# Optimization experiments

Measured on AMD Instinct MI355X. Metric: run time of the kernel, lower is better.

The kernel has to match this reference:

```python
import jax, jax.numpy as jnp
import numpy as np

# Intersection(mode='product'):
#   a_fk = a @ feats.T            # [Na, K]
#   b_fk = b @ feats.T            # [Nb, K]
#   mask = (a_fk[:,None,:] > 0) & (b_fk[None,:,:] > 0)
#   result = sum_k (a_fk[:,None,:] * b_fk[None,:,:]) * mask   # [Na, Nb]
# For the product op, (x*y)*[x>0 & y>0] == relu(x)*relu(y) elementwise
# (any term with a non-positive factor is zeroed either way), so the
# broadcast+mask+reduce collapses exactly into a GEMM over relu'd scores.

def setup_inputs() -> dict:
    key = jax.random.key(0)
    k1, k2, k3 = jax.random.split(key, 3)
    a = jax.random.normal(k1, (1024, 2048), dtype=jnp.float32)
    b = jax.random.normal(k2, (1024, 2048), dtype=jnp.float32)
    feats = jax.random.normal(k3, (128, 2048), dtype=jnp.float32)
    return {"a": a, "b": b, "feats": feats}

def reference(a, b, feats):
    a_fk = a @ feats.T            # [Na, K]
    b_fk = b @ feats.T            # [Nb, K]
    # masked product-intersection reduced over K; identical math to the
    # broadcast (Na, Nb, K) -> sum formulation of the torch module.
    return jnp.einsum('ak,bk->ab', jax.nn.relu(a_fk), jax.nn.relu(b_fk))
```

## Files before the change

### kernel.cpp

```cpp
#include <hip/hip_runtime.h>


typedef __attribute__((ext_vector_type(8))) __bf16 bf16x8;
typedef __attribute__((ext_vector_type(4))) __bf16 bf16x4;
typedef __attribute__((ext_vector_type(4))) float floatx4;

#define KD     2048
#define NF     128
#define NA     1024
#define NPART  8
#define KSL    256
#define FKN    (2048 * 128)

static __device__ inline bf16x4 cvt4(float4 u) {
    bf16x4 s;
    s[0] = (__bf16)u.x; s[1] = (__bf16)u.y; s[2] = (__bf16)u.z; s[3] = (__bf16)u.w;
    return s;
}

__global__ __launch_bounds__(256) void gemm1_part8(const float* __restrict__ A,
                                                   const float* __restrict__ B,
                                                   const float* __restrict__ F,
                                                   float* __restrict__ part) {
    __shared__ __bf16 Xs[32 * 72];
    __shared__ __bf16 Fs[128 * 72];

    const int t    = threadIdx.x;
    const int m0   = blockIdx.x * 32;
    const int s    = blockIdx.y;
    const int k0   = s * KSL;
    const float* src = (m0 < NA) ? (A + (size_t)m0 * KD)
                                 : (B + (size_t)(m0 - NA) * KD);

    const int lane = t & 63;
    const int w    = t >> 6;
    const int ln   = lane & 15;
    const int quad = lane >> 4;
    const int q8   = quad * 8;

    floatx4 acc[2][2];
#pragma unroll
    for (int mt = 0; mt < 2; mt++)
#pragma unroll
        for (int nt = 0; nt < 2; nt++)
            acc[mt][nt] = (floatx4){0.f, 0.f, 0.f, 0.f};

    const int srow = t >> 4;
    const int scol = (t & 15) * 4;
    const float* xp0 = src + (size_t)srow * KD        + (k0 + scol);
    const float* xp1 = src + (size_t)(srow + 16) * KD + (k0 + scol);
    const float* fp  = F   + (size_t)srow * KD        + (k0 + scol);

    float4 x0 = *(const float4*)(xp0);
    float4 x1 = *(const float4*)(xp1);
    float4 fa[8];
#pragma unroll
    for (int i = 0; i < 8; i++)
        fa[i] = *(const float4*)(fp + (size_t)i * 16 * KD);

#pragma unroll
    for (int kk = 0; kk < KSL; kk += 64) {
        *(bf16x4*)&Xs[srow * 72 + scol]        = cvt4(x0);
        *(bf16x4*)&Xs[(srow + 16) * 72 + scol] = cvt4(x1);
#pragma unroll
        for (int i = 0; i < 8; i++)
            *(bf16x4*)&Fs[(i * 16 + srow) * 72 + scol] = cvt4(fa[i]);
        __syncthreads();

        if (kk + 64 < KSL) {
            x0 = *(const float4*)(xp0 + kk + 64);
            x1 = *(const float4*)(xp1 + kk + 64);
#pragma unroll
            for (int i = 0; i < 8; i++)
                fa[i] = *(const float4*)(fp + (size_t)i * 16 * KD + kk + 64);
        }

#pragma unroll
        for (int sub = 0; sub < 64; sub += 32) {
            bf16x8 bfrag[2];
#pragma unroll
            for (int nt = 0; nt < 2; nt++)
                bfrag[nt] = *(const bf16x8*)&Fs[(w * 32 + nt * 16 + ln) * 72 + sub + q8];
#pragma unroll
            for (int mt = 0; mt < 2; mt++) {
                bf16x8 af = *(const bf16x8*)&Xs[(mt * 16 + ln) * 72 + sub + q8];
#pragma unroll
                for (int nt = 0; nt < 2; nt++)
                    acc[mt][nt] = __builtin_amdgcn_mfma_f32_16x16x32_bf16(
                        af, bfrag[nt], acc[mt][nt], 0, 0, 0);
            }
        }
        __syncthreads();
    }

    float* pdst = part + (size_t)s * FKN;
#pragma unroll
    for (int mt = 0; mt < 2; mt++)
#pragma unroll
        for (int nt = 0; nt < 2; nt++)
#pragma unroll
            for (int r = 0; r < 4; r++) {
                int row = m0 + mt * 16 + quad * 4 + r;
                int col = w * 32 + nt * 16 + ln;
                pdst[(size_t)row * NF + col] = acc[mt][nt][r];
            }
}

__global__ __launch_bounds__(256) void reduce_relu(const float* __restrict__ part,
                                                   __bf16* __restrict__ fkb) {
    int idx = blockIdx.x * 256 + threadIdx.x;
    size_t base = (size_t)idx * 4;
    float4 sum = make_float4(0.f, 0.f, 0.f, 0.f);
#pragma unroll
    for (int s = 0; s < NPART; s++) {
        float4 u = *(const float4*)(part + (size_t)s * FKN + base);
        sum.x += u.x; sum.y += u.y; sum.z += u.z; sum.w += u.w;
    }
    bf16x4 o;
    o[0] = (__bf16)fmaxf(sum.x, 0.f);
    o[1] = (__bf16)fmaxf(sum.y, 0.f);
    o[2] = (__bf16)fmaxf(sum.z, 0.f);
    o[3] = (__bf16)fmaxf(sum.w, 0.f);
    *(bf16x4*)(fkb + base) = o;
}

__global__ __launch_bounds__(256) void gemm2(const __bf16* __restrict__ fkb,
                                             float* __restrict__ out) {
    __shared__ __bf16 Ps[64 * 136];
    __shared__ __bf16 Qs[64 * 136];

    const int t    = threadIdx.x;
    const int i0   = blockIdx.y * 64;
    const int j0   = blockIdx.x * 64;
    const int lane = t & 63;
    const int w    = t >> 6;
    const int wm   = w & 1;
    const int wn   = w >> 1;
    const int ln   = lane & 15;
    const int quad = lane >> 4;
    const int q8   = quad * 8;

    const int prow = t >> 2, pcol = (t & 3) * 32;
    {
        const __bf16* p = fkb + (size_t)(i0 + prow) * NF + pcol;
        const __bf16* q = fkb + (size_t)(NA + j0 + prow) * NF + pcol;
#pragma unroll
        for (int c = 0; c < 32; c += 8) {
            *(bf16x8*)&Ps[prow * 136 + pcol + c] = *(const bf16x8*)(p + c);
            *(bf16x8*)&Qs[prow * 136 + pcol + c] = *(const bf16x8*)(q + c);
        }
    }
    __syncthreads();

    floatx4 acc[2][2];
#pragma unroll
    for (int mt = 0; mt < 2; mt++)
#pragma unroll
        for (int nt = 0; nt < 2; nt++)
            acc[mt][nt] = (floatx4){0.f, 0.f, 0.f, 0.f};

#pragma unroll
    for (int k0 = 0; k0 < 128; k0 += 32) {
        bf16x8 af[2], bf[2];
#pragma unroll
        for (int mt = 0; mt < 2; mt++)
            af[mt] = *(const bf16x8*)&Ps[(wm * 32 + mt * 16 + ln) * 136 + k0 + q8];
#pragma unroll
        for (int nt = 0; nt < 2; nt++)
            bf[nt] = *(const bf16x8*)&Qs[(wn * 32 + nt * 16 + ln) * 136 + k0 + q8];
#pragma unroll
        for (int mt = 0; mt < 2; mt++)
#pragma unroll
            for (int nt = 0; nt < 2; nt++)
                acc[mt][nt] = __builtin_amdgcn_mfma_f32_16x16x32_bf16(
                    af[mt], bf[nt], acc[mt][nt], 0, 0, 0);
    }

#pragma unroll
    for (int mt = 0; mt < 2; mt++)
#pragma unroll
        for (int nt = 0; nt < 2; nt++)
#pragma unroll
            for (int r = 0; r < 4; r++) {
                int row = i0 + wm * 32 + mt * 16 + quad * 4 + r;
                int col = j0 + wn * 32 + nt * 16 + ln;
                out[(size_t)row * 1024 + col] = acc[mt][nt][r];
            }
}

extern "C" void kernel_launch(void* const* d_in, const int* in_sizes, int n_in,
                              void* d_out, int out_size, void* d_ws, size_t ws_size,
                              hipStream_t stream) {
    const float* a     = (const float*)d_in[0];
    const float* b     = (const float*)d_in[1];
    const float* feats = (const float*)d_in[2];
    float* out = (float*)d_out;

    float*   part = (float*)d_ws;
    __bf16*  fkb  = (__bf16*)((char*)d_ws + (size_t)NPART * FKN * 4);

    gemm1_part8<<<dim3(64, NPART), 256, 0, stream>>>(a, b, feats, part);
    reduce_relu<<<256, 256, 0, stream>>>(part, fkb);
    gemm2<<<dim3(16, 16), 256, 0, stream>>>(fkb, out);
}
```

Before: 78.51 us.

## Stage full K-slice in shared memory with a single barrier and 64-row tiles

The first GEMM kernel now loads all four 64-wide K chunks into a four-stage shared-memory buffer before computing. This replaces the per-chunk sync-compute loop with a single barrier. The row tile doubles from 32 to 64, which halves the grid to 256 blocks and halves the redundant loads of the feats tile. In exchange, shared memory per block rises to about 110KB, which lowers occupancy. Register pressure also grows from two in-flight chunks and twice the accumulators, and fewer blocks may underfill the GPU's compute units.

Measured after the change: 77.91 us. Within noise of the previous version (-0.8%).

```diff
diff --git a/kernel.cpp b/kernel.cpp
--- a/kernel.cpp
+++ b/kernel.cpp
@@ -12,21 +12,50 @@
 #define KSL    256
 #define FKN    (2048 * 128)
 
+#define XSZ    (64 * 72)
+#define FSZ    (128 * 72)
+
 static __device__ inline bf16x4 cvt4(float4 u) {
     bf16x4 s;
     s[0] = (__bf16)u.x; s[1] = (__bf16)u.y; s[2] = (__bf16)u.z; s[3] = (__bf16)u.w;
     return s;
 }
 
-__global__ __launch_bounds__(256) void gemm1_part8(const float* __restrict__ A,
-                                                   const float* __restrict__ B,
-                                                   const float* __restrict__ F,
-                                                   float* __restrict__ part) {
-    __shared__ __bf16 Xs[32 * 72];
-    __shared__ __bf16 Fs[128 * 72];
+struct Chunk {
+    float4 x[4];
+    float4 f[8];
+};
+
+static __device__ inline void load_chunk(Chunk& ch, const float* xp,
+                                         const float* fp, int koff) {
+#pragma unroll
+    for (int j = 0; j < 4; j++)
+        ch.x[j] = *(const float4*)(xp + (size_t)j * 16 * KD + koff);
+#pragma unroll
+    for (int i = 0; i < 8; i++)
+        ch.f[i] = *(const float4*)(fp + (size_t)i * 16 * KD + koff);
+}
+
+static __device__ inline void write_chunk(const Chunk& ch, __bf16* Xc, __bf16* Fc,
+                                          int srow, int scol) {
+#pragma unroll
+    for (int j = 0; j < 4; j++)
+        *(bf16x4*)&Xc[(srow + 16 * j) * 72 + scol] = cvt4(ch.x[j]);
+#pragma unroll
+    for (int i = 0; i < 8; i++)
+        *(bf16x4*)&Fc[(srow + 16 * i) * 72 + scol] = cvt4(ch.f[i]);
+}
+
+__global__ __launch_bounds__(256) void gemm1_onebar(const float* __restrict__ A,
+                                                    const float* __restrict__ B,
+                                                    const float* __restrict__ F,
+                                                    float* __restrict__ part) {
+    __shared__ __attribute__((aligned(16))) __bf16 smem[4 * XSZ + 4 * FSZ];
+    __bf16* Xs = smem;
+    __bf16* Fs = smem + 4 * XSZ;
 
     const int t    = threadIdx.x;
-    const int m0   = blockIdx.x * 32;
+    const int m0   = blockIdx.x * 64;
     const int s    = blockIdx.y;
     const int k0   = s * KSL;
     const float* src = (m0 < NA) ? (A + (size_t)m0 * KD)
@@ -38,64 +67,53 @@
     const int quad = lane >> 4;
     const int q8   = quad * 8;
 
-    floatx4 acc[2][2];
-#pragma unroll
-    for (int mt = 0; mt < 2; mt++)
-#pragma unroll
-        for (int nt = 0; nt < 2; nt++)
-            acc[mt][nt] = (floatx4){0.f, 0.f, 0.f, 0.f};
-
     const int srow = t >> 4;
     const int scol = (t & 15) * 4;
-    const float* xp0 = src + (size_t)srow * KD        + (k0 + scol);
-    const float* xp1 = src + (size_t)(srow + 16) * KD + (k0 + scol);
-    const float* fp  = F   + (size_t)srow * KD        + (k0 + scol);
-
-    float4 x0 = *(const float4*)(xp0);
-    float4 x1 = *(const float4*)(xp1);
-    float4 fa[8];
-#pragma unroll
-    for (int i = 0; i < 8; i++)
-        fa[i] = *(const float4*)(fp + (size_t)i * 16 * KD);
-
-#pragma unroll
-    for (int kk = 0; kk < KSL; kk += 64) {
-        *(bf16x4*)&Xs[srow * 72 + scol]        = cvt4(x0);
-        *(bf16x4*)&Xs[(srow + 16) * 72 + scol] = cvt4(x1);
-#pragma unroll
-        for (int i = 0; i < 8; i++)
-            *(bf16x4*)&Fs[(i * 16 + srow) * 72 + scol] = cvt4(fa[i]);
-        __syncthreads();
-
-        if (kk + 64 < KSL) {
-            x0 = *(const float4*)(xp0 + kk + 64);
-            x1 = *(const float4*)(xp1 + kk + 64);
-#pragma unroll
-            for (int i = 0; i < 8; i++)
-                fa[i] = *(const float4*)(fp + (size_t)i * 16 * KD + kk + 64);
-        }
-
+    const float* xp = src + (size_t)srow * KD + (k0 + scol);
+    const float* fp = F   + (size_t)srow * KD + (k0 + scol);
+
+    Chunk ca, cb;
+    load_chunk(ca, xp, fp, 0);
+    load_chunk(cb, xp, fp, 64);
+    write_chunk(ca, Xs + 0 * XSZ, Fs + 0 * FSZ, srow, scol);
+    load_chunk(ca, xp, fp, 128);
+    write_chunk(cb, Xs + 1 * XSZ, Fs + 1 * FSZ, srow, scol);
+    load_chunk(cb, xp, fp, 192);
+    write_chunk(ca, Xs + 2 * XSZ, Fs + 2 * FSZ, srow, scol);
+    write_chunk(cb, Xs + 3 * XSZ, Fs + 3 * FSZ, srow, scol);
+    __syncthreads();
+
+    floatx4 acc[4][2];
+#pragma unroll
+    for (int mt = 0; mt < 4; mt++)
+#pragma unroll
+        for (int nt = 0; nt < 2; nt++)
+            acc[mt][nt] = (floatx4){0.f, 0.f, 0.f, 0.f};
+
+#pragma unroll
+    for (int c = 0; c < 4; c++) {
+        const __bf16* Xc = Xs + c * XSZ;
+        const __bf16* Fc = Fs + c * FSZ;
 #pragma unroll
         for (int sub = 0; sub < 64; sub += 32) {
             bf16x8 bfrag[2];
 #pragma unroll
             for (int nt = 0; nt < 2; nt++)
-                bfrag[nt] = *(const bf16x8*)&Fs[(w * 32 + nt * 16 + ln) * 72 + sub + q8];
-#pragma unroll
-            for (int mt = 0; mt < 2; mt++) {
-                bf16x8 af = *(const bf16x8*)&Xs[(mt * 16 + ln) * 72 + sub + q8];
+                bfrag[nt] = *(const bf16x8*)&Fc[(w * 32 + nt * 16 + ln) * 72 + sub + q8];
+#pragma unroll
+            for (int mt = 0; mt < 4; mt++) {
+                bf16x8 af = *(const bf16x8*)&Xc[(mt * 16 + ln) * 72 + sub + q8];
 #pragma unroll
                 for (int nt = 0; nt < 2; nt++)
                     acc[mt][nt] = __builtin_amdgcn_mfma_f32_16x16x32_bf16(
                         af, bfrag[nt], acc[mt][nt], 0, 0, 0);
             }
         }
-        __syncthreads();
     }
 
     float* pdst = part + (size_t)s * FKN;
 #pragma unroll
-    for (int mt = 0; mt < 2; mt++)
+    for (int mt = 0; mt < 4; mt++)
 #pragma unroll
         for (int nt = 0; nt < 2; nt++)
 #pragma unroll
@@ -199,7 +217,7 @@
     float*   part = (float*)d_ws;
     __bf16*  fkb  = (__bf16*)((char*)d_ws + (size_t)NPART * FKN * 4);
 
-    gemm1_part8<<<dim3(64, NPART), 256, 0, stream>>>(a, b, feats, part);
+    gemm1_onebar<<<dim3(32, NPART), 256, 0, stream>>>(a, b, feats, part);
     reduce_relu<<<256, 256, 0, stream>>>(part, fkb);
     gemm2<<<dim3(16, 16), 256, 0, stream>>>(fkb, out);
 }
```
